# Performance work log

Hardware: AMD Instinct MI355X
Metric: run time of the kernel (lower is better)

The kernel has to match this reference:

```python
import jax, jax.numpy as jnp
import numpy as np

MODEL_DIM = 1024
NUM_HEADS = 16
DIM_PER_HEAD = MODEL_DIM // NUM_HEADS
LN_EPS = 1e-5


def setup_inputs() -> dict:
    key = jax.random.key(0)
    ks = jax.random.split(key, 12)
    B, L, D = 4, 2048, MODEL_DIM
    s = 0.02
    return {
        "query": jax.random.normal(ks[0], (B, L, D), jnp.float32),
        "key": jax.random.normal(ks[1], (B, L, D), jnp.float32),
        "value": jax.random.normal(ks[2], (B, L, D), jnp.float32),
        "Wq": jax.random.normal(ks[3], (D, D), jnp.float32) * s,
        "bq": jnp.zeros((D,), jnp.float32),
        "Wk": jax.random.normal(ks[4], (D, D), jnp.float32) * s,
        "bk": jnp.zeros((D,), jnp.float32),
        "Wv": jax.random.normal(ks[5], (D, D), jnp.float32) * s,
        "bv": jnp.zeros((D,), jnp.float32),
        "Wo": jax.random.normal(ks[6], (D, D), jnp.float32) * s,
        "bo": jnp.zeros((D,), jnp.float32),
        "gamma": jnp.ones((D,), jnp.float32),
        "beta": jnp.zeros((D,), jnp.float32),
    }


def reference(query, key, value, Wq, bq, Wk, bk, Wv, bv, Wo, bo, gamma, beta):
    B, L, D = query.shape
    H, d = NUM_HEADS, DIM_PER_HEAD
    scale = d ** (-0.5)
    # torch nn.Linear: y = x @ W.T + b
    q = (query @ Wq.T + bq).reshape(B * H, L, d)  # faithful row-major view split
    k = (key @ Wk.T + bk).reshape(B * H, L, d)
    v = (value @ Wv.T + bv).reshape(B * H, L, d)
    atten = jnp.einsum('bqd,bkd->bqk', q, k) * scale  # [B*H, L, L]
    atten = jax.nn.softmax(atten, axis=2)
    # dropout: identity in eval mode
    context = jnp.einsum('bqk,bkd->bqd', atten, v).reshape(B, L, D)
    output = context @ Wo.T + bo
    x = query + output  # residual
    mu = jnp.mean(x, axis=-1, keepdims=True)
    var = jnp.var(x, axis=-1, keepdims=True)
    out = (x - mu) * jax.lax.rsqrt(var + LN_EPS) * gamma + beta
    return (out, atten)
```

## Files before the change

kernel.cpp:

```cpp
#include <hip/hip_runtime.h>
#include <cstdint>
#include <cstddef>

typedef _Float16 half8 __attribute__((ext_vector_type(8)));
typedef _Float16 half4 __attribute__((ext_vector_type(4)));
typedef __fp16 fp16x2 __attribute__((ext_vector_type(2)));
typedef float f32x4 __attribute__((ext_vector_type(4)));
typedef int int2v __attribute__((ext_vector_type(2)));

#define MFMA16(a, b, c) __builtin_amdgcn_mfma_f32_16x16x32_f16((a), (b), (c), 0, 0, 0)
#define MFMA16x16(a, b, c) __builtin_amdgcn_mfma_f32_16x16x16f16((a), (b), (c), 0, 0, 0)

__device__ __forceinline__ void gload_lds16(const void* g, void* l) {
  __builtin_amdgcn_global_load_lds(
      (const __attribute__((address_space(1))) void*)g,
      (__attribute__((address_space(3))) void*)l, 16, 0, 0);
}

__device__ __forceinline__ float fexp2(float x) {
#if __has_builtin(__builtin_amdgcn_exp2f)
  return __builtin_amdgcn_exp2f(x);
#else
  return exp2f(x);
#endif
}

__device__ __forceinline__ int cvtpk16(float a, float b) {
  fp16x2 h = __builtin_amdgcn_cvt_pkrtz(a, b);
  return __builtin_bit_cast(int, h);
}

__global__ __launch_bounds__(256) void cvt_f16(
    const float* __restrict__ q, const float* __restrict__ k, const float* __restrict__ v,
    const float* __restrict__ wq, const float* __restrict__ wk, const float* __restrict__ wv,
    _Float16* __restrict__ xq, _Float16* __restrict__ xk, _Float16* __restrict__ xv,
    _Float16* __restrict__ wq16, _Float16* __restrict__ wk16, _Float16* __restrict__ wv16)
{
  constexpr int S8 = 1048576;
  constexpr int W8 = 131072;
  int u = blockIdx.x * 256 + threadIdx.x;
  const float* src;
  _Float16* dst;
  if (u < S8) { src = q; dst = xq; }
  else if ((u -= S8) < S8) { src = k; dst = xk; }
  else if ((u -= S8) < S8) { src = v; dst = xv; }
  else if ((u -= S8) < W8) { src = wq; dst = wq16; }
  else if ((u -= W8) < W8) { src = wk; dst = wk16; }
  else { u -= W8; src = wv; dst = wv16; }
  const float4 f0 = reinterpret_cast<const float4*>(src)[u * 2];
  const float4 f1 = reinterpret_cast<const float4*>(src)[u * 2 + 1];
  half8 h;
  h[0] = (_Float16)f0.x; h[1] = (_Float16)f0.y; h[2] = (_Float16)f0.z; h[3] = (_Float16)f0.w;
  h[4] = (_Float16)f1.x; h[5] = (_Float16)f1.y; h[6] = (_Float16)f1.z; h[7] = (_Float16)f1.w;
  reinterpret_cast<half8*>(dst)[u] = h;
}

__global__ __launch_bounds__(256) void vtrans(
    const _Float16* __restrict__ v, _Float16* __restrict__ vt)
{
  __shared__ _Float16 T[64][72];
  const int g = blockIdx.y, kt = blockIdx.x;
  const int tid = threadIdx.x;
  const size_t gbase = (size_t)g * 131072;
  const int sr = tid >> 2, sc = (tid & 3) * 16;
  {
    const half8* src = reinterpret_cast<const half8*>(v + gbase + (size_t)(kt * 64 + sr) * 64 + sc);
    *reinterpret_cast<half8*>(&T[sr][sc]) = src[0];
    *reinterpret_cast<half8*>(&T[sr][sc + 8]) = src[1];
  }
  __syncthreads();
  const int d = tid >> 2, kc = (tid & 3) * 16;
  half8 h0, h1;
#pragma unroll
  for (int j = 0; j < 8; ++j) { h0[j] = T[kc + j][d]; h1[j] = T[kc + 8 + j][d]; }
  half8* dst = reinterpret_cast<half8*>(vt + gbase + (size_t)d * 2048 + kt * 64 + kc);
  dst[0] = h0;
  dst[1] = h1;
}

template <bool WF32, bool RES>
__global__ __launch_bounds__(256) void gemm128(
    const _Float16* __restrict__ A, const void* __restrict__ Wp,
    const float* __restrict__ bias, const float* __restrict__ resid,
    void* __restrict__ Out, int N, float scale)
{
  constexpr int K = 1024;
  __shared__ _Float16 As[128 * 64];
  __shared__ _Float16 Bs[128 * 64];
  const int tid = threadIdx.x;
  const int lane = tid & 63, w = tid >> 6;
  const int lo = lane & 15, hi = lane >> 4;
  const int wr = w >> 1, wc = w & 1;
  const int rbase = blockIdx.x * 128, cbase = blockIdx.y * 128;
  const int e0 = w * 512 + lane * 8;

  f32x4 acc[4][4];
#pragma unroll
  for (int m = 0; m < 4; ++m)
#pragma unroll
    for (int n = 0; n < 4; ++n) acc[m][n] = f32x4{0.f, 0.f, 0.f, 0.f};

  for (int kk = 0; kk < K; kk += 64) {
    __syncthreads();
#pragma unroll
    for (int i = 0; i < 4; ++i) {
      const int e = i * 2048 + e0;
      gload_lds16(A + (size_t)(rbase + (e >> 6)) * K + kk + (e & 63),
                  (char*)As + i * 4096 + w * 1024);
    }
    if constexpr (!WF32) {
#pragma unroll
      for (int i = 0; i < 4; ++i) {
        const int e = i * 2048 + e0;
        gload_lds16((const _Float16*)Wp + (size_t)(cbase + (e >> 6)) * K + kk + (e & 63),
                    (char*)Bs + i * 4096 + w * 1024);
      }
    } else {
#pragma unroll
      for (int i = 0; i < 4; ++i) {
        const int e = i * 2048 + e0;
        const float4* src = reinterpret_cast<const float4*>(
            (const float*)Wp + (size_t)(cbase + (e >> 6)) * K + kk + (e & 63));
        const float4 f0 = src[0], f1 = src[1];
        half8 h;
        h[0] = (_Float16)f0.x; h[1] = (_Float16)f0.y; h[2] = (_Float16)f0.z; h[3] = (_Float16)f0.w;
        h[4] = (_Float16)f1.x; h[5] = (_Float16)f1.y; h[6] = (_Float16)f1.z; h[7] = (_Float16)f1.w;
        *reinterpret_cast<half8*>(Bs + e) = h;
      }
    }
    __syncthreads();
#pragma unroll
    for (int k0 = 0; k0 < 2; ++k0) {
      half8 a[4], b[4];
#pragma unroll
      for (int m = 0; m < 4; ++m)
        a[m] = *reinterpret_cast<const half8*>(As + (wr * 64 + m * 16 + lo) * 64 + k0 * 32 + hi * 8);
#pragma unroll
      for (int n = 0; n < 4; ++n)
        b[n] = *reinterpret_cast<const half8*>(Bs + (wc * 64 + n * 16 + lo) * 64 + k0 * 32 + hi * 8);
#pragma unroll
      for (int m = 0; m < 4; ++m)
#pragma unroll
        for (int n = 0; n < 4; ++n) acc[m][n] = MFMA16(a[m], b[n], acc[m][n]);
    }
  }
#pragma unroll
  for (int m = 0; m < 4; ++m) {
#pragma unroll
    for (int n = 0; n < 4; ++n) {
      const int col = cbase + wc * 64 + n * 16 + lo;
      const float bv = bias[col];
#pragma unroll
      for (int r = 0; r < 4; ++r) {
        const int row = rbase + wr * 64 + m * 16 + hi * 4 + r;
        float v = acc[m][n][r] + bv;
        if constexpr (RES) {
          v += resid[(size_t)row * 1024 + col];
          ((float*)Out)[(size_t)row * N + col] = v;
        } else {
          ((_Float16*)Out)[(size_t)row * N + col] = (_Float16)(v * scale);
        }
      }
    }
  }
}

__global__ __launch_bounds__(512) void attn_fused(
    const _Float16* __restrict__ qg, const _Float16* __restrict__ kg,
    const _Float16* __restrict__ vtg, _Float16* __restrict__ ctx,
    float* __restrict__ attnp)
{
  __shared__ _Float16 Kt[2][128 * 64];
  __shared__ _Float16 Vt[2][64 * 128];
  __shared__ float Ps[8 * 2048];
  const int tid = threadIdx.x;
  const int lane = tid & 63, w = tid >> 6;
  const int lo = lane & 15, hi = lane >> 4;
  const int bid = blockIdx.x;
  const int g = bid & 63;
  const int q0 = (bid >> 6) * 256;
  const size_t gbase = (size_t)g * (2048 * 64);

  const int eK0 = tid * 8, eK1 = 4096 + tid * 8;
  const int kr0 = eK0 >> 6, kc0 = (eK0 & 63) ^ ((kr0 & 7) << 3);
  const int kr1 = eK1 >> 6, kc1 = (eK1 & 63) ^ ((kr1 & 7) << 3);
  const int vr0 = eK0 >> 7, vc0 = (eK0 & 127) ^ ((vr0 & 7) << 3);
  const int vr1 = eK1 >> 7, vc1 = (eK1 & 127) ^ ((vr1 & 7) << 3);

  float* ab = attnp + (size_t)g * 2048 * 2048;
  const _Float16* vtb = vtg + (size_t)g * (64 * 2048);
  float* Pw = Ps + w * 2048;

  half8 qf[2][2];
#pragma unroll
  for (int m = 0; m < 2; ++m)
#pragma unroll
    for (int k0 = 0; k0 < 2; ++k0)
      qf[m][k0] = *reinterpret_cast<const half8*>(
          qg + gbase + (size_t)(q0 + w * 32 + m * 16 + lo) * 64 + k0 * 32 + hi * 8);

  float ls[2] = {0.f, 0.f};

  gload_lds16(kg + gbase + (size_t)kr0 * 64 + kc0, (char*)Kt[0] + w * 1024);
  gload_lds16(kg + gbase + (size_t)kr1 * 64 + kc1, (char*)Kt[0] + 8192 + w * 1024);

  for (int kt = 0; kt < 16; ++kt) {
    const int cur = kt & 1;
    __syncthreads();
    if (kt < 15) {
      const _Float16* kn = kg + gbase + (size_t)(kt + 1) * (128 * 64);
      gload_lds16(kn + (size_t)kr0 * 64 + kc0, (char*)Kt[cur ^ 1] + w * 1024);
      gload_lds16(kn + (size_t)kr1 * 64 + kc1, (char*)Kt[cur ^ 1] + 8192 + w * 1024);
    }
    f32x4 s[2][8];
#pragma unroll
    for (int m = 0; m < 2; ++m)
#pragma unroll
      for (int n = 0; n < 8; ++n) s[m][n] = f32x4{0.f, 0.f, 0.f, 0.f};
#pragma unroll
    for (int k0 = 0; k0 < 2; ++k0) {
      half8 b[8];
#pragma unroll
      for (int n = 0; n < 8; ++n) {
        const int row = n * 16 + lo;
        b[n] = *reinterpret_cast<const half8*>(
            Kt[cur] + row * 64 + ((k0 * 32 + hi * 8) ^ ((row & 7) << 3)));
      }
#pragma unroll
      for (int m = 0; m < 2; ++m)
#pragma unroll
        for (int n = 0; n < 8; ++n) s[m][n] = MFMA16(b[n], qf[m][k0], s[m][n]);
    }
#pragma unroll
    for (int m = 0; m < 2; ++m) {
      float t = 0.f;
#pragma unroll
      for (int nb = 0; nb < 8; ++nb)
#pragma unroll
        for (int r = 0; r < 4; ++r) t += fexp2(s[m][nb][r]);
      ls[m] += t;
    }
  }

  float dr[2];
#pragma unroll
  for (int m = 0; m < 2; ++m) {
    float t = ls[m];
    t += __shfl_xor(t, 16, 64);
    t += __shfl_xor(t, 32, 64);
    dr[m] = __log2f(t);
  }

  f32x4 o[2][4];
#pragma unroll
  for (int m = 0; m < 2; ++m)
#pragma unroll
    for (int n = 0; n < 4; ++n) o[m][n] = f32x4{0.f, 0.f, 0.f, 0.f};

  gload_lds16(kg + gbase + (size_t)kr0 * 64 + kc0, (char*)Kt[0] + w * 1024);
  gload_lds16(kg + gbase + (size_t)kr1 * 64 + kc1, (char*)Kt[0] + 8192 + w * 1024);
  gload_lds16(vtb + (size_t)vr0 * 2048 + vc0, (char*)Vt[0] + w * 1024);
  gload_lds16(vtb + (size_t)vr1 * 2048 + vc1, (char*)Vt[0] + 8192 + w * 1024);

  for (int kt = 0; kt < 16; ++kt) {
    const int cur = kt & 1;
    if (kt == 0) asm volatile("s_waitcnt vmcnt(0) lgkmcnt(0)" ::: "memory");
    else asm volatile("s_waitcnt vmcnt(16) lgkmcnt(0)" ::: "memory");
    __builtin_amdgcn_s_barrier();
    __builtin_amdgcn_sched_barrier(0);
    if (kt < 15) {
      const _Float16* kn = kg + gbase + (size_t)(kt + 1) * (128 * 64);
      const _Float16* vn = vtb + (kt + 1) * 128;
      gload_lds16(kn + (size_t)kr0 * 64 + kc0, (char*)Kt[cur ^ 1] + w * 1024);
      gload_lds16(kn + (size_t)kr1 * 64 + kc1, (char*)Kt[cur ^ 1] + 8192 + w * 1024);
      gload_lds16(vn + (size_t)vr0 * 2048 + vc0, (char*)Vt[cur ^ 1] + w * 1024);
      gload_lds16(vn + (size_t)vr1 * 2048 + vc1, (char*)Vt[cur ^ 1] + 8192 + w * 1024);
    }
    __builtin_amdgcn_sched_barrier(0);
    f32x4 s[2][8];
#pragma unroll
    for (int m = 0; m < 2; ++m)
#pragma unroll
      for (int n = 0; n < 8; ++n) s[m][n] = f32x4{-dr[m], -dr[m], -dr[m], -dr[m]};
#pragma unroll
    for (int k0 = 0; k0 < 2; ++k0) {
      half8 b[8];
#pragma unroll
      for (int n = 0; n < 8; ++n) {
        const int row = n * 16 + lo;
        b[n] = *reinterpret_cast<const half8*>(
            Kt[cur] + row * 64 + ((k0 * 32 + hi * 8) ^ ((row & 7) << 3)));
      }
#pragma unroll
      for (int m = 0; m < 2; ++m)
#pragma unroll
        for (int n = 0; n < 8; ++n) s[m][n] = MFMA16(b[n], qf[m][k0], s[m][n]);
    }
#pragma unroll
    for (int m = 0; m < 2; ++m) {
      int pk[8][2];
#pragma unroll
      for (int nb = 0; nb < 8; ++nb) {
        const float p0 = fexp2(s[m][nb][0]);
        const float p1 = fexp2(s[m][nb][1]);
        const float p2 = fexp2(s[m][nb][2]);
        const float p3 = fexp2(s[m][nb][3]);
        pk[nb][0] = cvtpk16(p0, p1);
        pk[nb][1] = cvtpk16(p2, p3);
        const f32x4 f = {p0, p1, p2, p3};
        *reinterpret_cast<f32x4*>(
            Pw + lo * 128 + ((nb * 16 + hi * 4) ^ ((lo & 7) << 2))) = f;
      }
      asm volatile("s_waitcnt lgkmcnt(0)" ::: "memory");
#pragma unroll
      for (int i = 0; i < 8; ++i) {
        const int rl = i * 2 + (lane >> 5);
        const int klo = (lane & 31) * 4;
        const f32x4 f = *reinterpret_cast<const f32x4*>(
            Pw + rl * 128 + (klo ^ ((rl & 7) << 2)));
        __builtin_nontemporal_store(
            f, reinterpret_cast<f32x4*>(
                   ab + (size_t)(q0 + w * 32 + m * 16 + rl) * 2048 + kt * 128 + klo));
      }
      asm volatile("s_waitcnt lgkmcnt(0)" ::: "memory");
#pragma unroll
      for (int nb = 0; nb < 8; ++nb) {
        half4 vb[4];
#pragma unroll
        for (int n = 0; n < 4; ++n) {
          const int d = n * 16 + lo;
          vb[n] = *reinterpret_cast<const half4*>(
              Vt[cur] + d * 128 + ((nb * 16 + hi * 4) ^ ((d & 7) << 3)));
        }
        const int2v t2 = {pk[nb][0], pk[nb][1]};
        const half4 pa = __builtin_bit_cast(half4, t2);
#pragma unroll
        for (int n = 0; n < 4; ++n) o[m][n] = MFMA16x16(pa, vb[n], o[m][n]);
      }
    }
  }
#pragma unroll
  for (int m = 0; m < 2; ++m)
#pragma unroll
    for (int n = 0; n < 4; ++n)
#pragma unroll
      for (int r = 0; r < 4; ++r)
        ctx[gbase + (size_t)(q0 + w * 32 + m * 16 + hi * 4 + r) * 64 + n * 16 + lo] =
            (_Float16)o[m][n][r];
}

__global__ __launch_bounds__(256) void ln_kernel(
    float* __restrict__ x, const float* __restrict__ gamma, const float* __restrict__ beta)
{
  const int row = blockIdx.x;
  const int t = threadIdx.x;
  float4 v = *reinterpret_cast<float4*>(x + (size_t)row * 1024 + t * 4);
  float s = v.x + v.y + v.z + v.w;
  float ss = v.x * v.x + v.y * v.y + v.z * v.z + v.w * v.w;
#pragma unroll
  for (int off = 1; off < 64; off <<= 1) {
    s += __shfl_xor(s, off, 64);
    ss += __shfl_xor(ss, off, 64);
  }
  __shared__ float sm[8];
  const int wv = t >> 6, ln = t & 63;
  if (ln == 0) { sm[wv] = s; sm[4 + wv] = ss; }
  __syncthreads();
  s = sm[0] + sm[1] + sm[2] + sm[3];
  ss = sm[4] + sm[5] + sm[6] + sm[7];
  const float mu = s * (1.0f / 1024.0f);
  const float var = ss * (1.0f / 1024.0f) - mu * mu;
  const float rstd = rsqrtf(var + 1e-5f);
  const float4 gv = *reinterpret_cast<const float4*>(gamma + t * 4);
  const float4 bv = *reinterpret_cast<const float4*>(beta + t * 4);
  v.x = (v.x - mu) * rstd * gv.x + bv.x;
  v.y = (v.y - mu) * rstd * gv.y + bv.y;
  v.z = (v.z - mu) * rstd * gv.z + bv.z;
  v.w = (v.w - mu) * rstd * gv.w + bv.w;
  *reinterpret_cast<float4*>(x + (size_t)row * 1024 + t * 4) = v;
}

extern "C" void kernel_launch(void* const* d_in, const int* in_sizes, int n_in,
                              void* d_out, int out_size, void* d_ws, size_t ws_size,
                              hipStream_t stream) {
  const float* query = (const float*)d_in[0];
  const float* key_ = (const float*)d_in[1];
  const float* value = (const float*)d_in[2];
  const float* Wq = (const float*)d_in[3];
  const float* bq = (const float*)d_in[4];
  const float* Wk = (const float*)d_in[5];
  const float* bk = (const float*)d_in[6];
  const float* Wv = (const float*)d_in[7];
  const float* bv = (const float*)d_in[8];
  const float* Wo = (const float*)d_in[9];
  const float* bo = (const float*)d_in[10];
  const float* gamma = (const float*)d_in[11];
  const float* beta = (const float*)d_in[12];

  float* out = (float*)d_out;
  float* attnp = out + (size_t)8192 * 1024;

  _Float16* xq = (_Float16*)attnp;
  _Float16* xk = xq + (size_t)8388608;
  _Float16* xv = xk + (size_t)8388608;
  _Float16* wq16 = xv + (size_t)8388608;
  _Float16* wk16 = wq16 + (size_t)1048576;
  _Float16* wv16 = wk16 + (size_t)1048576;

  _Float16* vt = (_Float16*)out;

  _Float16* qb = (_Float16*)d_ws;
  _Float16* kb2 = qb + (size_t)8388608;
  _Float16* vb2 = kb2 + (size_t)8388608;
  _Float16* ctx = vb2;

  constexpr float QSCALE = 0.125f * 1.44269504088896f;

  cvt_f16<<<dim3(13824), dim3(256), 0, stream>>>(query, key_, value, Wq, Wk, Wv,
                                                 xq, xk, xv, wq16, wk16, wv16);
  gemm128<false, false><<<dim3(64, 8), dim3(256), 0, stream>>>(xq, wq16, bq, nullptr, qb, 1024, QSCALE);
  gemm128<false, false><<<dim3(64, 8), dim3(256), 0, stream>>>(xk, wk16, bk, nullptr, kb2, 1024, 1.0f);
  gemm128<false, false><<<dim3(64, 8), dim3(256), 0, stream>>>(xv, wv16, bv, nullptr, vb2, 1024, 1.0f);
  vtrans<<<dim3(32, 64), dim3(256), 0, stream>>>(vb2, vt);
  attn_fused<<<dim3(512), dim3(512), 0, stream>>>(qb, kb2, vt, ctx, attnp);
  gemm128<true, true><<<dim3(64, 8), dim3(256), 0, stream>>>(ctx, Wo, bo, query, out, 1024, 1.0f);
  ln_kernel<<<dim3(8192), dim3(256), 0, stream>>>(out, gamma, beta);
}
```

Before: 454.7 us.

## Split attention key tile into halves and shrink P staging buffer for occupancy

Each 128-key tile in both attention passes is now processed as two 64-key halves, so fewer score registers are live at once. The per-wave LDS staging buffer for the fp32 probability write-out shrinks from 2048 to 256 floats, and the write-out is done in four 4-row chunks. Together with a launch_bounds minimum-blocks hint, this aims to cut register and LDS pressure so more blocks fit per CU. In exchange the write-out has more LDS round trips and waitcnt stalls, plus divergent per-chunk writes.

```diff
diff --git a/kernel.cpp b/kernel.cpp
--- a/kernel.cpp
+++ b/kernel.cpp
@@ -165,14 +165,14 @@
   }
 }
 
-__global__ __launch_bounds__(512) void attn_fused(
+__global__ __launch_bounds__(512, 4) void attn_fused(
     const _Float16* __restrict__ qg, const _Float16* __restrict__ kg,
     const _Float16* __restrict__ vtg, _Float16* __restrict__ ctx,
     float* __restrict__ attnp)
 {
   __shared__ _Float16 Kt[2][128 * 64];
   __shared__ _Float16 Vt[2][64 * 128];
-  __shared__ float Ps[8 * 2048];
+  __shared__ float Ps[8 * 256];
   const int tid = threadIdx.x;
   const int lane = tid & 63, w = tid >> 6;
   const int lo = lane & 15, hi = lane >> 4;
@@ -189,7 +189,7 @@
 
   float* ab = attnp + (size_t)g * 2048 * 2048;
   const _Float16* vtb = vtg + (size_t)g * (64 * 2048);
-  float* Pw = Ps + w * 2048;
+  float* Pw = Ps + w * 256;
 
   half8 qf[2][2];
 #pragma unroll
@@ -212,33 +212,33 @@
       gload_lds16(kn + (size_t)kr0 * 64 + kc0, (char*)Kt[cur ^ 1] + w * 1024);
       gload_lds16(kn + (size_t)kr1 * 64 + kc1, (char*)Kt[cur ^ 1] + 8192 + w * 1024);
     }
-    f32x4 s[2][8];
-#pragma unroll
-    for (int m = 0; m < 2; ++m)
-#pragma unroll
-      for (int n = 0; n < 8; ++n) s[m][n] = f32x4{0.f, 0.f, 0.f, 0.f};
-#pragma unroll
-    for (int k0 = 0; k0 < 2; ++k0) {
-      half8 b[8];
-#pragma unroll
-      for (int n = 0; n < 8; ++n) {
-        const int row = n * 16 + lo;
-        b[n] = *reinterpret_cast<const half8*>(
-            Kt[cur] + row * 64 + ((k0 * 32 + hi * 8) ^ ((row & 7) << 3)));
-      }
+#pragma unroll
+    for (int h = 0; h < 2; ++h) {
+      f32x4 s[2][4];
 #pragma unroll
       for (int m = 0; m < 2; ++m)
 #pragma unroll
-        for (int n = 0; n < 8; ++n) s[m][n] = MFMA16(b[n], qf[m][k0], s[m][n]);
-    }
-#pragma unroll
-    for (int m = 0; m < 2; ++m) {
-      float t = 0.f;
-#pragma unroll
-      for (int nb = 0; nb < 8; ++nb)
-#pragma unroll
-        for (int r = 0; r < 4; ++r) t += fexp2(s[m][nb][r]);
-      ls[m] += t;
+        for (int j = 0; j < 4; ++j) s[m][j] = f32x4{0.f, 0.f, 0.f, 0.f};
+#pragma unroll
+      for (int k0 = 0; k0 < 2; ++k0) {
+#pragma unroll
+        for (int j = 0; j < 4; ++j) {
+          const int row = (h * 4 + j) * 16 + lo;
+          const half8 b = *reinterpret_cast<const half8*>(
+              Kt[cur] + row * 64 + ((k0 * 32 + hi * 8) ^ ((row & 7) << 3)));
+          s[0][j] = MFMA16(b, qf[0][k0], s[0][j]);
+          s[1][j] = MFMA16(b, qf[1][k0], s[1][j]);
+        }
+      }
+#pragma unroll
+      for (int m = 0; m < 2; ++m) {
+        float t = 0.f;
+#pragma unroll
+        for (int j = 0; j < 4; ++j)
+#pragma unroll
+          for (int r = 0; r < 4; ++r) t += fexp2(s[m][j][r]);
+        ls[m] += t;
+      }
     }
   }
 
@@ -277,54 +277,66 @@
       gload_lds16(vn + (size_t)vr1 * 2048 + vc1, (char*)Vt[cur ^ 1] + 8192 + w * 1024);
     }
     __builtin_amdgcn_sched_barrier(0);
-    f32x4 s[2][8];
-#pragma unroll
-    for (int m = 0; m < 2; ++m)
-#pragma unroll
-      for (int n = 0; n < 8; ++n) s[m][n] = f32x4{-dr[m], -dr[m], -dr[m], -dr[m]};
-#pragma unroll
-    for (int k0 = 0; k0 < 2; ++k0) {
-      half8 b[8];
-#pragma unroll
-      for (int n = 0; n < 8; ++n) {
-        const int row = n * 16 + lo;
-        b[n] = *reinterpret_cast<const half8*>(
-            Kt[cur] + row * 64 + ((k0 * 32 + hi * 8) ^ ((row & 7) << 3)));
-      }
+#pragma unroll
+    for (int h = 0; h < 2; ++h) {
+      f32x4 s[2][4];
 #pragma unroll
       for (int m = 0; m < 2; ++m)
 #pragma unroll
-        for (int n = 0; n < 8; ++n) s[m][n] = MFMA16(b[n], qf[m][k0], s[m][n]);
-    }
-#pragma unroll
-    for (int m = 0; m < 2; ++m) {
-      int pk[8][2];
-#pragma unroll
-      for (int nb = 0; nb < 8; ++nb) {
-        const float p0 = fexp2(s[m][nb][0]);
-        const float p1 = fexp2(s[m][nb][1]);
-        const float p2 = fexp2(s[m][nb][2]);
-        const float p3 = fexp2(s[m][nb][3]);
-        pk[nb][0] = cvtpk16(p0, p1);
-        pk[nb][1] = cvtpk16(p2, p3);
-        const f32x4 f = {p0, p1, p2, p3};
-        *reinterpret_cast<f32x4*>(
-            Pw + lo * 128 + ((nb * 16 + hi * 4) ^ ((lo & 7) << 2))) = f;
-      }
-      asm volatile("s_waitcnt lgkmcnt(0)" ::: "memory");
-#pragma unroll
-      for (int i = 0; i < 8; ++i) {
-        const int rl = i * 2 + (lane >> 5);
-        const int klo = (lane & 31) * 4;
-        const f32x4 f = *reinterpret_cast<const f32x4*>(
-            Pw + rl * 128 + (klo ^ ((rl & 7) << 2)));
-        __builtin_nontemporal_store(
-            f, reinterpret_cast<f32x4*>(
-                   ab + (size_t)(q0 + w * 32 + m * 16 + rl) * 2048 + kt * 128 + klo));
-      }
-      asm volatile("s_waitcnt lgkmcnt(0)" ::: "memory");
-#pragma unroll
-      for (int nb = 0; nb < 8; ++nb) {
+        for (int j = 0; j < 4; ++j) s[m][j] = f32x4{-dr[m], -dr[m], -dr[m], -dr[m]};
+#pragma unroll
+      for (int k0 = 0; k0 < 2; ++k0) {
+#pragma unroll
+        for (int j = 0; j < 4; ++j) {
+          const int row = (h * 4 + j) * 16 + lo;
+          const half8 b = *reinterpret_cast<const half8*>(
+              Kt[cur] + row * 64 + ((k0 * 32 + hi * 8) ^ ((row & 7) << 3)));
+          s[0][j] = MFMA16(b, qf[0][k0], s[0][j]);
+          s[1][j] = MFMA16(b, qf[1][k0], s[1][j]);
+        }
+      }
+      int pk[2][4][2];
+#pragma unroll
+      for (int m = 0; m < 2; ++m)
+#pragma unroll
+        for (int j = 0; j < 4; ++j) {
+          const float p0 = fexp2(s[m][j][0]);
+          const float p1 = fexp2(s[m][j][1]);
+          const float p2 = fexp2(s[m][j][2]);
+          const float p3 = fexp2(s[m][j][3]);
+          pk[m][j][0] = cvtpk16(p0, p1);
+          pk[m][j][1] = cvtpk16(p2, p3);
+          s[m][j] = f32x4{p0, p1, p2, p3};
+        }
+      const int myc = lo >> 2;
+      const int lo3 = lo & 3;
+#pragma unroll
+      for (int m = 0; m < 2; ++m) {
+#pragma unroll
+        for (int c = 0; c < 4; ++c) {
+          if (myc == c) {
+#pragma unroll
+            for (int j = 0; j < 4; ++j)
+              *reinterpret_cast<f32x4*>(
+                  Pw + lo3 * 64 + ((j * 16 + hi * 4) ^ (lo3 << 4))) = s[m][j];
+          }
+          asm volatile("s_waitcnt lgkmcnt(0)" ::: "memory");
+          {
+            const int rl = lane >> 4;
+            const int klo = (lane & 15) * 4;
+            const f32x4 f = *reinterpret_cast<const f32x4*>(
+                Pw + rl * 64 + (klo ^ (rl << 4)));
+            __builtin_nontemporal_store(
+                f, reinterpret_cast<f32x4*>(
+                       ab + (size_t)(q0 + w * 32 + m * 16 + c * 4 + rl) * 2048 +
+                       kt * 128 + h * 64 + klo));
+          }
+          asm volatile("s_waitcnt lgkmcnt(0)" ::: "memory");
+        }
+      }
+#pragma unroll
+      for (int j = 0; j < 4; ++j) {
+        const int nb = h * 4 + j;
         half4 vb[4];
 #pragma unroll
         for (int n = 0; n < 4; ++n) {
@@ -332,10 +344,13 @@
           vb[n] = *reinterpret_cast<const half4*>(
               Vt[cur] + d * 128 + ((nb * 16 + hi * 4) ^ ((d & 7) << 3)));
         }
-        const int2v t2 = {pk[nb][0], pk[nb][1]};
-        const half4 pa = __builtin_bit_cast(half4, t2);
-#pragma unroll
-        for (int n = 0; n < 4; ++n) o[m][n] = MFMA16x16(pa, vb[n], o[m][n]);
+#pragma unroll
+        for (int m = 0; m < 2; ++m) {
+          const int2v t2 = {pk[m][j][0], pk[m][j][1]};
+          const half4 pa = __builtin_bit_cast(half4, t2);
+#pragma unroll
+          for (int n = 0; n < 4; ++n) o[m][n] = MFMA16x16(pa, vb[n], o[m][n]);
+        }
       }
     }
   }
```

After: 531.4 us. 1.17x slower.
